# Kernel optimization log

Measured on AMD Instinct MI355X. Metric: run time of the kernel, lower is better.

The kernel has to match this reference:

```python
import jax, jax.numpy as jnp
import numpy as np

DIM = 1024
HEADS = 16
HEAD_DIM = DIM // HEADS
B, N = 2, 2048


def setup_inputs() -> dict:
    key = jax.random.key(0)
    k1, k2, k3, k4 = jax.random.split(key, 4)
    x = jax.random.normal(k1, (B, N, DIM), dtype=jnp.float32)
    # torch Linear weights: shape (out_features, in_features), y = x @ W.T + b
    w_qkv = jax.random.normal(k2, (3 * DIM, DIM), dtype=jnp.float32) * (DIM ** -0.5)
    w_proj = jax.random.normal(k3, (DIM, DIM), dtype=jnp.float32) * (DIM ** -0.5)
    b_proj = jax.random.normal(k4, (DIM,), dtype=jnp.float32) * 0.01
    return {"x": x, "w_qkv": w_qkv, "w_proj": w_proj, "b_proj": b_proj}


def reference(x, w_qkv, w_proj, b_proj):
    Bb, Nn, D = x.shape
    scale = HEAD_DIM ** -0.5
    qkv = x @ w_qkv.T                                # [B, N, 3D]
    qkv = qkv.reshape(Bb, Nn, 3, HEADS, HEAD_DIM)
    qkv = jnp.transpose(qkv, (2, 0, 3, 1, 4))        # [3, B, H, N, hd]
    q, k, v = qkv[0], qkv[1], qkv[2]
    attn = jnp.einsum('bhqd,bhkd->bhqk', q, k) * scale
    attn = jax.nn.softmax(attn, axis=-1)
    out = jnp.einsum('bhqk,bhkd->bhqd', attn, v)     # [B, H, N, hd]
    out = jnp.transpose(out, (0, 2, 1, 3)).reshape(Bb, Nn, D)
    return out @ w_proj.T + b_proj
```

## Files before the change

### kernel.cpp

```cpp
#include <hip/hip_runtime.h>
#include <cstdint>
#include <cstddef>

using u16 = unsigned short;
using u32 = uint32_t;
using f32x4  = __attribute__((ext_vector_type(4))) float;
using bf16x8 = __attribute__((ext_vector_type(8))) __bf16;
using s16x4  = __attribute__((ext_vector_type(4))) short;

#define D_MODEL 1024
#define N_HEADS 16
#define HD      64
#define SEQ     2048
#define QKV_LD  3072
#define K2SCALE 0.18033688011112042f

__device__ __forceinline__ u16 f2b(float f) {
  union { float f; u32 u; } v; v.f = f;
  u32 r = 0x7FFFu + ((v.u >> 16) & 1u);
  return (u16)((v.u + r) >> 16);
}

__device__ __forceinline__ u32 pkbf16(float a, float b) {
  return (u32)f2b(a) | ((u32)f2b(b) << 16);
}

#define MFMA16(A, B, C) __builtin_amdgcn_mfma_f32_16x16x16bf16_1k(A, B, C, 0, 0, 0)

__device__ __forceinline__ void gld16(const u16* g, u16* l) {
  __builtin_amdgcn_global_load_lds(
      (const __attribute__((address_space(1))) void*)g,
      (__attribute__((address_space(3))) void*)l, 16, 0, 0);
}

__global__ void cast3_bf16(const float* __restrict__ x, const float* __restrict__ wq,
                           const float* __restrict__ wp, u16* __restrict__ dst) {
  int i = blockIdx.x * blockDim.x + threadIdx.x;
  const float* src;
  int off;
  if (blockIdx.x < 4096)      { src = x;  off = 0; }
  else if (blockIdx.x < 7168) { src = wq; off = 4096 * 256; }
  else                        { src = wp; off = 7168 * 256; }
  float4 f = ((const float4*)src)[i - off];
  ushort4 o;
  o.x = f2b(f.x); o.y = f2b(f.y); o.z = f2b(f.z); o.w = f2b(f.w);
  ((ushort4*)dst)[i] = o;
}

template<int OUTMODE, int MT>
__launch_bounds__(256, 3)
__global__ void gemm_nt(const u16* __restrict__ A, const u16* __restrict__ B,
                        u16* __restrict__ Ob, float* __restrict__ Of,
                        const float* __restrict__ bias, int N, int K) {
  __shared__ __attribute__((aligned(16))) u16 sA[2][MT * 32];
  __shared__ __attribute__((aligned(16))) u16 sB[2][128 * 32];

  const int tid  = threadIdx.x;
  const int lane = tid & 63;
  const int w    = tid >> 6;
  const int qd   = lane >> 4;
  const int ln   = lane & 15;
  constexpr int MI = MT / 32;
  const int wm   = (w >> 1) * (MT / 2);
  const int wn   = (w & 1) * 64;
  const int m0   = blockIdx.y * MT;
  const int n0   = blockIdx.x * 128;

  auto stage = [&](int kk, int buf) {
    int k0 = kk * 32;
    #pragma unroll
    for (int c = 0; c < MT / 64; ++c) {
      int sbase = w * MT + c * 64;
      int s = sbase + lane;
      int row = s >> 2, col = (s & 3) * 8;
      gld16(A + (size_t)(m0 + row) * K + k0 + col, &sA[buf][sbase * 8]);
    }
    #pragma unroll
    for (int c = 0; c < 2; ++c) {
      int sbase = w * 128 + c * 64;
      int s = sbase + lane;
      int row = s >> 2, col = (s & 3) * 8;
      gld16(B + (size_t)(n0 + row) * K + k0 + col, &sB[buf][sbase * 8]);
    }
  };

  f32x4 acc[MI][4] = {};
  const int NK = K >> 5;
  stage(0, 0);

  for (int kk = 0; kk < NK; ++kk) {
    const int cur = kk & 1;
    __syncthreads();
    if (kk + 1 < NK) stage(kk + 1, cur ^ 1);

    bf16x8 af[MI], bfm[4];
    #pragma unroll
    for (int i = 0; i < MI; ++i)
      af[i] = *(const bf16x8*)&sA[cur][(wm + i * 16 + ln) * 32 + qd * 8];
    #pragma unroll
    for (int j = 0; j < 4; ++j)
      bfm[j] = *(const bf16x8*)&sB[cur][(wn + j * 16 + ln) * 32 + qd * 8];
    #pragma unroll
    for (int i = 0; i < MI; ++i)
      #pragma unroll
      for (int j = 0; j < 4; ++j)
        acc[i][j] = __builtin_amdgcn_mfma_f32_16x16x32_bf16(af[i], bfm[j], acc[i][j], 0, 0, 0);
  }

  #pragma unroll
  for (int i = 0; i < MI; ++i) {
    #pragma unroll
    for (int j = 0; j < 4; ++j) {
      #pragma unroll
      for (int r = 0; r < 4; ++r) {
        int row = m0 + wm + i * 16 + qd * 4 + r;
        int col = n0 + wn + j * 16 + ln;
        float v = acc[i][j][r];
        if (OUTMODE == 0) {
          if (col < D_MODEL) v *= K2SCALE;
          Ob[(size_t)row * N + col] = f2b(v);
        } else {
          Of[(size_t)row * N + col] = v + bias[col];
        }
      }
    }
  }
}

__launch_bounds__(256, 2)
__global__ void attn_kernel(const u16* __restrict__ qkv, u16* __restrict__ outb) {
  __shared__ __attribute__((aligned(16))) u16 sK[2][2][128 * 32];
  __shared__ __attribute__((aligned(16))) u32 sVT[2][64 * 64];

  const int tid  = threadIdx.x;
  const int lane = tid & 63;
  const int w    = tid >> 6;
  const int qd   = lane >> 4;
  const int ln   = lane & 15;
  const int qp   = blockIdx.x;
  const int h    = blockIdx.y & 15;
  const int b    = blockIdx.y >> 4;
  const size_t tokbase = (size_t)b * SEQ;
  const int q0   = qp * 128;
  const int qoff = h * HD;
  const int koff = D_MODEL + h * HD;
  const int voff = 2 * D_MODEL + h * HD;

  bf16x8 aq[2][2];
  #pragma unroll
  for (int c2 = 0; c2 < 2; ++c2)
    #pragma unroll
    for (int hf = 0; hf < 2; ++hf)
      aq[c2][hf] = *(const bf16x8*)(qkv + (tokbase + q0 + c2 * 64 + w * 16 + ln) * QKV_LD
                                    + qoff + hf * 32 + qd * 8);

  auto stageK = [&](int kt, int buf) {
    #pragma unroll
    for (int hf = 0; hf < 2; ++hf)
      #pragma unroll
      for (int c = 0; c < 2; ++c) {
        int sbase = w * 128 + c * 64;
        int s = sbase + lane;
        int row = s >> 2, col = (s & 3) * 8;
        gld16(qkv + (tokbase + kt * 128 + row) * QKV_LD + koff + hf * 32 + col,
              &sK[buf][hf][sbase * 8]);
      }
  };
  auto loadV = [&](int kt, uint4* va, uint4* vb) {
    #pragma unroll
    for (int it = 0; it < 2; ++it) {
      int j = it * 256 + tid;
      int tp = j & 63, d0 = (j >> 6) * 8;
      const u16* g0 = qkv + (tokbase + kt * 128 + tp * 2) * QKV_LD + voff + d0;
      va[it] = *(const uint4*)g0;
      vb[it] = *(const uint4*)(g0 + QKV_LD);
    }
  };
  auto writeV = [&](int buf, const uint4* va, const uint4* vb) {
    #pragma unroll
    for (int it = 0; it < 2; ++it) {
      int j = it * 256 + tid;
      int tp = j & 63, d0 = (j >> 6) * 8;
      const u32* a  = (const u32*)&va[it];
      const u32* bb = (const u32*)&vb[it];
      #pragma unroll
      for (int e = 0; e < 4; ++e) {
        sVT[buf][(d0 + 2 * e    ) * 64 + (tp ^ (e << 4)      )] =
            __builtin_amdgcn_perm(bb[e], a[e], 0x05040100u);
        sVT[buf][(d0 + 2 * e + 1) * 64 + (tp ^ (e << 4) ^ 8  )] =
            __builtin_amdgcn_perm(bb[e], a[e], 0x07060302u);
      }
    }
  };

  stageK(0, 0);
  uint4 va[2], vb[2];
  loadV(0, va, vb);
  writeV(0, va, vb);
  loadV(1, va, vb);

  f32x4 accOT[2][4] = {};
  float psum[2] = {0.f, 0.f};
  const int tsw = (ln & 7) << 3;

  for (int kt = 0; kt < 16; ++kt) {
    const int cur = kt & 1, nxt = cur ^ 1;
    __syncthreads();
    if (kt < 15) { stageK(kt + 1, nxt); writeV(nxt, va, vb); }
    if (kt < 14) { loadV(kt + 2, va, vb); }

    #pragma unroll
    for (int cb = 0; cb < 8; ++cb) {
      bf16x8 ak0 = *(const bf16x8*)&sK[cur][0][(cb * 16 + ln) * 32 + qd * 8];
      bf16x8 ak1 = *(const bf16x8*)&sK[cur][1][(cb * 16 + ln) * 32 + qd * 8];
      f32x4 st[2];
      #pragma unroll
      for (int c2 = 0; c2 < 2; ++c2) {
        f32x4 z = {0.f, 0.f, 0.f, 0.f};
        f32x4 t = __builtin_amdgcn_mfma_f32_16x16x32_bf16(ak0, aq[c2][0], z, 0, 0, 0);
        st[c2]  = __builtin_amdgcn_mfma_f32_16x16x32_bf16(ak1, aq[c2][1], t, 0, 0, 0);
      }
      s16x4 pf[2];
      #pragma unroll
      for (int c2 = 0; c2 < 2; ++c2) {
        float p0 = __builtin_amdgcn_exp2f(st[c2][0]);
        float p1 = __builtin_amdgcn_exp2f(st[c2][1]);
        float p2 = __builtin_amdgcn_exp2f(st[c2][2]);
        float p3 = __builtin_amdgcn_exp2f(st[c2][3]);
        psum[c2] += (p0 + p1) + (p2 + p3);
        union { u32 d[2]; s16x4 v; } pk;
        pk.d[0] = pkbf16(p0, p1);
        pk.d[1] = pkbf16(p2, p3);
        pf[c2] = pk.v;
      }
      #pragma unroll
      for (int ob = 0; ob < 4; ++ob) {
        s16x4 vf = *(const s16x4*)&sVT[cur][(ob * 16 + ln) * 64
                                           + ((cb * 8 + qd * 2) ^ tsw)];
        accOT[0][ob] = MFMA16(vf, pf[0], accOT[0][ob]);
        accOT[1][ob] = MFMA16(vf, pf[1], accOT[1][ob]);
      }
    }
  }

  #pragma unroll
  for (int c2 = 0; c2 < 2; ++c2) {
    float s = psum[c2];
    s += __shfl_xor(s, 16, 64);
    s += __shfl_xor(s, 32, 64);
    psum[c2] = 1.0f / s;
  }

  u16* sOut = (u16*)&sK[0][0][0];
  __syncthreads();
  #pragma unroll
  for (int c2 = 0; c2 < 2; ++c2)
    #pragma unroll
    for (int ob = 0; ob < 4; ++ob) {
      u32 lo = pkbf16(accOT[c2][ob][0] * psum[c2], accOT[c2][ob][1] * psum[c2]);
      u32 hi = pkbf16(accOT[c2][ob][2] * psum[c2], accOT[c2][ob][3] * psum[c2]);
      ((u32*)sOut)[(c2 * 64 + w * 16 + ln) * 36 + ob * 8 + qd * 2    ] = lo;
      ((u32*)sOut)[(c2 * 64 + w * 16 + ln) * 36 + ob * 8 + qd * 2 + 1] = hi;
    }
  __syncthreads();
  #pragma unroll
  for (int it = 0; it < 4; ++it) {
    int idx = it * 256 + tid;
    int token = idx >> 3, chunk = idx & 7;
    uint4 v = *(const uint4*)&sOut[token * 72 + chunk * 8];
    *(uint4*)&outb[(tokbase + q0 + token) * D_MODEL + h * HD + chunk * 8] = v;
  }
}

extern "C" void kernel_launch(void* const* d_in, const int* in_sizes, int n_in,
                              void* d_out, int out_size, void* d_ws, size_t ws_size,
                              hipStream_t stream) {
  const float* x      = (const float*)d_in[0];
  const float* w_qkv  = (const float*)d_in[1];
  const float* w_proj = (const float*)d_in[2];
  const float* b_proj = (const float*)d_in[3];
  float* out = (float*)d_out;

  u16* ws     = (u16*)d_ws;
  u16* xb     = ws;
  u16* wqkvb  = xb    + (size_t)4096 * 1024;
  u16* wprojb = wqkvb + (size_t)3072 * 1024;
  u16* qkvb   = wprojb + (size_t)1024 * 1024;
  u16* attnb  = qkvb  + (size_t)4096 * 3072;

  cast3_bf16<<<8192, 256, 0, stream>>>(x, w_qkv, w_proj, xb);

  gemm_nt<0, 128><<<dim3(24, 32), 256, 0, stream>>>(xb, wqkvb, qkvb, nullptr, nullptr, 3072, 1024);

  attn_kernel<<<dim3(16, 32), 256, 0, stream>>>(qkvb, attnb);

  gemm_nt<1, 64><<<dim3(8, 64), 256, 0, stream>>>(attnb, wprojb, nullptr, out, b_proj, 1024, 1024);
}
```

Before: 197.6 us.

## Load K fragments directly from global into registers, drop K shared staging

Instead of staging K tiles into LDS via async global-to-LDS loads, each lane now loads its K MFMA fragments straight from global memory into a register array, prefetching the next tile's fragment right after each use. This removes the K LDS buffer and its reads, cutting shared memory use, and launch bounds are raised to 3 blocks per SM to exploit that. The cost is more VGPRs (64 extra per lane for K fragments) under a tighter register cap, which risks spills. Global loads are also less coalesced, since each lane reads 16-byte chunks from rows spaced by the QKV stride.

```diff
diff --git a/kernel.cpp b/kernel.cpp
--- a/kernel.cpp
+++ b/kernel.cpp
@@ -127,9 +127,8 @@
   }
 }
 
-__launch_bounds__(256, 2)
+__launch_bounds__(256, 3)
 __global__ void attn_kernel(const u16* __restrict__ qkv, u16* __restrict__ outb) {
-  __shared__ __attribute__((aligned(16))) u16 sK[2][2][128 * 32];
   __shared__ __attribute__((aligned(16))) u32 sVT[2][64 * 64];
 
   const int tid  = threadIdx.x;
@@ -154,18 +153,8 @@
       aq[c2][hf] = *(const bf16x8*)(qkv + (tokbase + q0 + c2 * 64 + w * 16 + ln) * QKV_LD
                                     + qoff + hf * 32 + qd * 8);
 
-  auto stageK = [&](int kt, int buf) {
-    #pragma unroll
-    for (int hf = 0; hf < 2; ++hf)
-      #pragma unroll
-      for (int c = 0; c < 2; ++c) {
-        int sbase = w * 128 + c * 64;
-        int s = sbase + lane;
-        int row = s >> 2, col = (s & 3) * 8;
-        gld16(qkv + (tokbase + kt * 128 + row) * QKV_LD + koff + hf * 32 + col,
-              &sK[buf][hf][sbase * 8]);
-      }
-  };
+  const u16* kfbase = qkv + tokbase * QKV_LD + koff + qd * 8;
+
   auto loadV = [&](int kt, uint4* va, uint4* vb) {
     #pragma unroll
     for (int it = 0; it < 2; ++it) {
@@ -185,15 +174,21 @@
       const u32* bb = (const u32*)&vb[it];
       #pragma unroll
       for (int e = 0; e < 4; ++e) {
-        sVT[buf][(d0 + 2 * e    ) * 64 + (tp ^ (e << 4)      )] =
+        sVT[buf][(d0 + 2 * e    ) * 64 + (tp ^ (e << 4)    )] =
             __builtin_amdgcn_perm(bb[e], a[e], 0x05040100u);
-        sVT[buf][(d0 + 2 * e + 1) * 64 + (tp ^ (e << 4) ^ 8  )] =
+        sVT[buf][(d0 + 2 * e + 1) * 64 + (tp ^ (e << 4) ^ 8)] =
             __builtin_amdgcn_perm(bb[e], a[e], 0x07060302u);
       }
     }
   };
 
-  stageK(0, 0);
+  bf16x8 ck[8][2];
+  #pragma unroll
+  for (int cb = 0; cb < 8; ++cb) {
+    const u16* r = kfbase + (size_t)(cb * 16 + ln) * QKV_LD;
+    ck[cb][0] = *(const bf16x8*)r;
+    ck[cb][1] = *(const bf16x8*)(r + 32);
+  }
   uint4 va[2], vb[2];
   loadV(0, va, vb);
   writeV(0, va, vb);
@@ -204,21 +199,24 @@
   const int tsw = (ln & 7) << 3;
 
   for (int kt = 0; kt < 16; ++kt) {
-    const int cur = kt & 1, nxt = cur ^ 1;
+    const int cur = kt & 1;
     __syncthreads();
-    if (kt < 15) { stageK(kt + 1, nxt); writeV(nxt, va, vb); }
+    if (kt < 15) { writeV(cur ^ 1, va, vb); }
     if (kt < 14) { loadV(kt + 2, va, vb); }
 
     #pragma unroll
     for (int cb = 0; cb < 8; ++cb) {
-      bf16x8 ak0 = *(const bf16x8*)&sK[cur][0][(cb * 16 + ln) * 32 + qd * 8];
-      bf16x8 ak1 = *(const bf16x8*)&sK[cur][1][(cb * 16 + ln) * 32 + qd * 8];
       f32x4 st[2];
       #pragma unroll
       for (int c2 = 0; c2 < 2; ++c2) {
         f32x4 z = {0.f, 0.f, 0.f, 0.f};
-        f32x4 t = __builtin_amdgcn_mfma_f32_16x16x32_bf16(ak0, aq[c2][0], z, 0, 0, 0);
-        st[c2]  = __builtin_amdgcn_mfma_f32_16x16x32_bf16(ak1, aq[c2][1], t, 0, 0, 0);
+        f32x4 t = __builtin_amdgcn_mfma_f32_16x16x32_bf16(ck[cb][0], aq[c2][0], z, 0, 0, 0);
+        st[c2]  = __builtin_amdgcn_mfma_f32_16x16x32_bf16(ck[cb][1], aq[c2][1], t, 0, 0, 0);
+      }
+      if (kt < 15) {
+        const u16* r = kfbase + (size_t)((kt + 1) * 128 + cb * 16 + ln) * QKV_LD;
+        ck[cb][0] = *(const bf16x8*)r;
+        ck[cb][1] = *(const bf16x8*)(r + 32);
       }
       s16x4 pf[2];
       #pragma unroll
@@ -251,7 +249,7 @@
     psum[c2] = 1.0f / s;
   }
 
-  u16* sOut = (u16*)&sK[0][0][0];
+  u16* sOut = (u16*)&sVT[0][0];
   __syncthreads();
   #pragma unroll
   for (int c2 = 0; c2 < 2; ++c2)
```

New measurement: 349.9 us. +77.0%, slower.

## Split attention work across 512 threads with one query tile per wave

Applied to the files above, without the earlier changes.

The attention kernel now launches 512 threads per block (8 waves) instead of 256. Each wave handles 16 query rows instead of 32, which halves per-thread accumulators, Q fragments and softmax sums. K/V staging is spread across the larger thread count. The aim is more waves in flight to hide LDS and global latency and lower register pressure. In exchange, each K/V tile loaded from LDS is reused across fewer MFMAs per wave, and every barrier now synchronizes more waves.

```diff
diff --git a/kernel.cpp b/kernel.cpp
--- a/kernel.cpp
+++ b/kernel.cpp
@@ -127,7 +127,7 @@
   }
 }
 
-__launch_bounds__(256, 2)
+__launch_bounds__(512, 4)
 __global__ void attn_kernel(const u16* __restrict__ qkv, u16* __restrict__ outb) {
   __shared__ __attribute__((aligned(16))) u16 sK[2][2][128 * 32];
   __shared__ __attribute__((aligned(16))) u32 sVT[2][64 * 64];
@@ -146,61 +146,48 @@
   const int koff = D_MODEL + h * HD;
   const int voff = 2 * D_MODEL + h * HD;
 
-  bf16x8 aq[2][2];
-  #pragma unroll
-  for (int c2 = 0; c2 < 2; ++c2)
-    #pragma unroll
-    for (int hf = 0; hf < 2; ++hf)
-      aq[c2][hf] = *(const bf16x8*)(qkv + (tokbase + q0 + c2 * 64 + w * 16 + ln) * QKV_LD
-                                    + qoff + hf * 32 + qd * 8);
+  bf16x8 aq[2];
+  #pragma unroll
+  for (int hf = 0; hf < 2; ++hf)
+    aq[hf] = *(const bf16x8*)(qkv + (tokbase + q0 + w * 16 + ln) * QKV_LD
+                              + qoff + hf * 32 + qd * 8);
 
   auto stageK = [&](int kt, int buf) {
     #pragma unroll
-    for (int hf = 0; hf < 2; ++hf)
-      #pragma unroll
-      for (int c = 0; c < 2; ++c) {
-        int sbase = w * 128 + c * 64;
-        int s = sbase + lane;
-        int row = s >> 2, col = (s & 3) * 8;
-        gld16(qkv + (tokbase + kt * 128 + row) * QKV_LD + koff + hf * 32 + col,
-              &sK[buf][hf][sbase * 8]);
-      }
-  };
-  auto loadV = [&](int kt, uint4* va, uint4* vb) {
-    #pragma unroll
-    for (int it = 0; it < 2; ++it) {
-      int j = it * 256 + tid;
-      int tp = j & 63, d0 = (j >> 6) * 8;
-      const u16* g0 = qkv + (tokbase + kt * 128 + tp * 2) * QKV_LD + voff + d0;
-      va[it] = *(const uint4*)g0;
-      vb[it] = *(const uint4*)(g0 + QKV_LD);
-    }
-  };
-  auto writeV = [&](int buf, const uint4* va, const uint4* vb) {
-    #pragma unroll
-    for (int it = 0; it < 2; ++it) {
-      int j = it * 256 + tid;
-      int tp = j & 63, d0 = (j >> 6) * 8;
-      const u32* a  = (const u32*)&va[it];
-      const u32* bb = (const u32*)&vb[it];
-      #pragma unroll
-      for (int e = 0; e < 4; ++e) {
-        sVT[buf][(d0 + 2 * e    ) * 64 + (tp ^ (e << 4)      )] =
-            __builtin_amdgcn_perm(bb[e], a[e], 0x05040100u);
-        sVT[buf][(d0 + 2 * e + 1) * 64 + (tp ^ (e << 4) ^ 8  )] =
-            __builtin_amdgcn_perm(bb[e], a[e], 0x07060302u);
-      }
+    for (int hf = 0; hf < 2; ++hf) {
+      int s = w * 64 + lane;
+      int row = s >> 2, col = (s & 3) * 8;
+      gld16(qkv + (tokbase + kt * 128 + row) * QKV_LD + koff + hf * 32 + col,
+            &sK[buf][hf][w * 512]);
+    }
+  };
+  auto loadV = [&](int kt, uint4& va, uint4& vb) {
+    int tp = tid & 63, d0 = (tid >> 6) * 8;
+    const u16* g0 = qkv + (tokbase + kt * 128 + tp * 2) * QKV_LD + voff + d0;
+    va = *(const uint4*)g0;
+    vb = *(const uint4*)(g0 + QKV_LD);
+  };
+  auto writeV = [&](int buf, const uint4& va, const uint4& vb) {
+    int tp = tid & 63, d0 = (tid >> 6) * 8;
+    const u32* a  = (const u32*)&va;
+    const u32* bb = (const u32*)&vb;
+    #pragma unroll
+    for (int e = 0; e < 4; ++e) {
+      sVT[buf][(d0 + 2 * e    ) * 64 + (tp ^ (e << 4)    )] =
+          __builtin_amdgcn_perm(bb[e], a[e], 0x05040100u);
+      sVT[buf][(d0 + 2 * e + 1) * 64 + (tp ^ (e << 4) ^ 8)] =
+          __builtin_amdgcn_perm(bb[e], a[e], 0x07060302u);
     }
   };
 
   stageK(0, 0);
-  uint4 va[2], vb[2];
+  uint4 va, vb;
   loadV(0, va, vb);
   writeV(0, va, vb);
   loadV(1, va, vb);
 
-  f32x4 accOT[2][4] = {};
-  float psum[2] = {0.f, 0.f};
+  f32x4 accOT[4] = {};
+  float psum = 0.0f;
   const int tsw = (ln & 7) << 3;
 
   for (int kt = 0; kt < 16; ++kt) {
@@ -213,59 +200,45 @@
     for (int cb = 0; cb < 8; ++cb) {
       bf16x8 ak0 = *(const bf16x8*)&sK[cur][0][(cb * 16 + ln) * 32 + qd * 8];
       bf16x8 ak1 = *(const bf16x8*)&sK[cur][1][(cb * 16 + ln) * 32 + qd * 8];
-      f32x4 st[2];
-      #pragma unroll
-      for (int c2 = 0; c2 < 2; ++c2) {
-        f32x4 z = {0.f, 0.f, 0.f, 0.f};
-        f32x4 t = __builtin_amdgcn_mfma_f32_16x16x32_bf16(ak0, aq[c2][0], z, 0, 0, 0);
-        st[c2]  = __builtin_amdgcn_mfma_f32_16x16x32_bf16(ak1, aq[c2][1], t, 0, 0, 0);
-      }
-      s16x4 pf[2];
-      #pragma unroll
-      for (int c2 = 0; c2 < 2; ++c2) {
-        float p0 = __builtin_amdgcn_exp2f(st[c2][0]);
-        float p1 = __builtin_amdgcn_exp2f(st[c2][1]);
-        float p2 = __builtin_amdgcn_exp2f(st[c2][2]);
-        float p3 = __builtin_amdgcn_exp2f(st[c2][3]);
-        psum[c2] += (p0 + p1) + (p2 + p3);
-        union { u32 d[2]; s16x4 v; } pk;
-        pk.d[0] = pkbf16(p0, p1);
-        pk.d[1] = pkbf16(p2, p3);
-        pf[c2] = pk.v;
-      }
+      f32x4 z = {0.f, 0.f, 0.f, 0.f};
+      f32x4 t  = __builtin_amdgcn_mfma_f32_16x16x32_bf16(ak0, aq[0], z, 0, 0, 0);
+      f32x4 st = __builtin_amdgcn_mfma_f32_16x16x32_bf16(ak1, aq[1], t, 0, 0, 0);
+
+      float p0 = __builtin_amdgcn_exp2f(st[0]);
+      float p1 = __builtin_amdgcn_exp2f(st[1]);
+      float p2 = __builtin_amdgcn_exp2f(st[2]);
+      float p3 = __builtin_amdgcn_exp2f(st[3]);
+      psum += (p0 + p1) + (p2 + p3);
+      union { u32 d[2]; s16x4 v; } pk;
+      pk.d[0] = pkbf16(p0, p1);
+      pk.d[1] = pkbf16(p2, p3);
+
       #pragma unroll
       for (int ob = 0; ob < 4; ++ob) {
         s16x4 vf = *(const s16x4*)&sVT[cur][(ob * 16 + ln) * 64
                                            + ((cb * 8 + qd * 2) ^ tsw)];
-        accOT[0][ob] = MFMA16(vf, pf[0], accOT[0][ob]);
-        accOT[1][ob] = MFMA16(vf, pf[1], accOT[1][ob]);
+        accOT[ob] = MFMA16(vf, pk.v, accOT[ob]);
       }
     }
   }
 
-  #pragma unroll
-  for (int c2 = 0; c2 < 2; ++c2) {
-    float s = psum[c2];
-    s += __shfl_xor(s, 16, 64);
-    s += __shfl_xor(s, 32, 64);
-    psum[c2] = 1.0f / s;
-  }
-
-  u16* sOut = (u16*)&sK[0][0][0];
+  psum += __shfl_xor(psum, 16, 64);
+  psum += __shfl_xor(psum, 32, 64);
+  const float rinv = 1.0f / psum;
+
+  u16* sOut = (u16*)&sVT[0][0];
   __syncthreads();
   #pragma unroll
-  for (int c2 = 0; c2 < 2; ++c2)
-    #pragma unroll
-    for (int ob = 0; ob < 4; ++ob) {
-      u32 lo = pkbf16(accOT[c2][ob][0] * psum[c2], accOT[c2][ob][1] * psum[c2]);
-      u32 hi = pkbf16(accOT[c2][ob][2] * psum[c2], accOT[c2][ob][3] * psum[c2]);
-      ((u32*)sOut)[(c2 * 64 + w * 16 + ln) * 36 + ob * 8 + qd * 2    ] = lo;
-      ((u32*)sOut)[(c2 * 64 + w * 16 + ln) * 36 + ob * 8 + qd * 2 + 1] = hi;
-    }
+  for (int ob = 0; ob < 4; ++ob) {
+    u32 lo = pkbf16(accOT[ob][0] * rinv, accOT[ob][1] * rinv);
+    u32 hi = pkbf16(accOT[ob][2] * rinv, accOT[ob][3] * rinv);
+    ((u32*)sOut)[(w * 16 + ln) * 36 + ob * 8 + qd * 2    ] = lo;
+    ((u32*)sOut)[(w * 16 + ln) * 36 + ob * 8 + qd * 2 + 1] = hi;
+  }
   __syncthreads();
   #pragma unroll
-  for (int it = 0; it < 4; ++it) {
-    int idx = it * 256 + tid;
+  for (int it = 0; it < 2; ++it) {
+    int idx = it * 512 + tid;
     int token = idx >> 3, chunk = idx & 7;
     uint4 v = *(const uint4*)&sOut[token * 72 + chunk * 8];
     *(uint4*)&outb[(tokbase + q0 + token) * D_MODEL + h * HD + chunk * 8] = v;
@@ -292,7 +265,7 @@
 
   gemm_nt<0, 128><<<dim3(24, 32), 256, 0, stream>>>(xb, wqkvb, qkvb, nullptr, nullptr, 3072, 1024);
 
-  attn_kernel<<<dim3(16, 32), 256, 0, stream>>>(qkvb, attnb);
+  attn_kernel<<<dim3(16, 32), 512, 0, stream>>>(qkvb, attnb);
 
   gemm_nt<1, 64><<<dim3(8, 64), 256, 0, stream>>>(attnb, wprojb, nullptr, out, b_proj, 1024, 1024);
 }
```

After: 221.6 us. 12.1% more time.
